# Optimization experiments

Measured on AMD Instinct MI355X. Metric: run time of the kernel, lower is better.

The kernel has to match this reference:

```python
import jax, jax.numpy as jnp
from jax import lax
import numpy as np

B, T, D = 16, 4096, 512          # batch, encoder length, d_model
C, FW = 10, 100                  # aconv_chans, aconv_filts (kernel width 2*FW+1)
SHARP = 2.0                      # sharpening_factor


def setup_inputs() -> dict:
    key = jax.random.key(0)
    ks = jax.random.split(key, 11)
    s = 1.0 / np.sqrt(D)
    sc = 1.0 / np.sqrt(2 * FW + 1)
    return {
        "value": jax.random.normal(ks[0], (B, T, D), jnp.float32),
        "query": jax.random.normal(ks[1], (B, D), jnp.float32),
        "input_lengths": jax.random.randint(ks[2], (B,), T // 2, T + 1),
        "att_prev": jax.random.uniform(ks[3], (B, T), jnp.float32),
        # learned parameters (torch Linear stores W as [out,in]; y = x @ W.T + b)
        "W_enc": jax.random.uniform(ks[4], (D, D), jnp.float32, -s, s),
        "b_enc": jax.random.uniform(ks[5], (D,), jnp.float32, -s, s),
        "W_dec": jax.random.uniform(ks[6], (D, D), jnp.float32, -s, s),
        "W_att": jax.random.uniform(ks[7], (D, C), jnp.float32, -s, s),
        "W_conv": jax.random.uniform(ks[8], (C, 1, 2 * FW + 1), jnp.float32, -sc, sc),
        "w_g": jax.random.uniform(ks[9], (1, D), jnp.float32, -s, s),
        "b_g": jax.random.uniform(ks[10], (1,), jnp.float32, -s, s),
    }


def reference(value, query, input_lengths, att_prev,
              W_enc, b_enc, W_dec, W_att, W_conv, w_g, b_g):
    # pre_compute_enc_h = mlp_enc(enc_h): [B,T,D]
    pre_enc = jnp.einsum('btd,ed->bte', value, W_enc) + b_enc
    # dec_z_tiled = mlp_dec(dec_z): [B,1,D]
    dec_tiled = (query @ W_dec.T)[:, None, :]
    # loc_conv: 1D conv over T, in_ch=1 -> out_ch=C, same padding -> [B,C,T]
    conv = lax.conv_general_dilated(att_prev[:, None, :], W_conv,
                                    window_strides=(1,), padding=[(FW, FW)],
                                    dimension_numbers=('NCH', 'OIH', 'NCH'))
    # mlp_att on transposed conv: [B,T,C] @ W_att.T -> [B,T,D]
    att_conv = jnp.einsum('bct,dc->btd', conv, W_att)
    # e = gvec(tanh(sum)): [B,T]
    e = jnp.einsum('btd,d->bt', jnp.tanh(att_conv + pre_enc + dec_tiled), w_g[0]) + b_g[0]
    # pad mask: positions >= length are masked to -inf (use large finite neg)
    pad_mask = jnp.arange(T)[None, :] >= input_lengths[:, None]
    e = jnp.where(pad_mask, -1e30, e)
    att_weights = jax.nn.softmax(SHARP * e, axis=1)            # [B,T]
    context = jnp.einsum('btd,bt->bd', value, att_weights)     # [B,D]
    return context, att_weights
```

## Files before the change

### kernel.cpp

```cpp
#include <hip/hip_runtime.h>
#include <hip/hip_bf16.h>

constexpr int kB  = 16;
constexpr int kT  = 4096;
constexpr int kD  = 512;
constexpr int kC  = 10;
constexpr int kFW = 100;
constexpr int kKW = 2 * kFW + 1;
constexpr int kKP = 544;

typedef __attribute__((ext_vector_type(8))) short short8_t;
typedef __attribute__((ext_vector_type(4))) float float4_t;

__device__ __forceinline__ float tanh_fast(float x) {
  float ax = fabsf(x);
  float z  = __expf(-2.0f * ax);
  float r  = (1.0f - z) / (1.0f + z);
  return copysignf(r, x);
}

__device__ __forceinline__ short f2bf(float x) {
  unsigned u = __float_as_uint(x);
  u += 0x7fffu + ((u >> 16) & 1u);
  return (short)(u >> 16);
}

__device__ __forceinline__ unsigned pk2(float lo, float hi) {
  __hip_bfloat162 h = __float22bfloat162_rn(make_float2(lo, hi));
  union { __hip_bfloat162 h2; unsigned u; } cv; cv.h2 = h; return cv.u;
}

__device__ __forceinline__ float bf2f(short s) {
  return __uint_as_float(((unsigned)(unsigned short)s) << 16);
}

__device__ __forceinline__ void glds16(const void* g, void* l) {
  __builtin_amdgcn_global_load_lds(
      (const __attribute__((address_space(1))) void*)g,
      (__attribute__((address_space(3))) void*)l, 16, 0, 0);
}

__global__ __launch_bounds__(256) void prep_kernel(
    const float* __restrict__ query, const float* __restrict__ W_dec,
    const float* __restrict__ b_enc, float* __restrict__ bias,
    const float* __restrict__ W_enc, const float* __restrict__ W_att,
    short* __restrict__ Wbf,
    const float* __restrict__ att_prev, const float* __restrict__ W_conv,
    const float* __restrict__ value, const int* __restrict__ lens,
    short* __restrict__ Abf) {
  __shared__ float ap[256 + 2 * kFW];
  __shared__ float wc[kC * kKW];
  int blk = blockIdx.x;
  int tid = threadIdx.x;

  if (blk < 2048) {
    int gw   = (blk * 256 + tid) >> 6;
    int lane = tid & 63;
    int b = gw >> 9, d = gw & (kD - 1);
    const float* q = query + (size_t)b * kD;
    const float* w = W_dec + (size_t)d * kD;
    float s = 0.f;
#pragma unroll
    for (int k0 = 0; k0 < kD; k0 += 256) {
      float4 qa = *(const float4*)(q + k0 + lane * 4);
      float4 wa = *(const float4*)(w + k0 + lane * 4);
      s += qa.x * wa.x + qa.y * wa.y + qa.z * wa.z + qa.w * wa.w;
    }
#pragma unroll
    for (int off = 32; off > 0; off >>= 1) s += __shfl_down(s, off, 64);
    if (lane == 0) bias[gw] = b_enc[d] + s;
  } else if (blk < 2048 + 512) {
    int d = blk - 2048;
    for (int c = tid; c < kKP; c += 256) {
      float v = 0.f;
      if (c < kD)           v = W_enc[(size_t)d * kD + c];
      else if (c < kD + kC) v = W_att[(size_t)d * kC + (c - kD)];
      Wbf[(size_t)d * kKP + c] = f2bf(v);
    }
  } else if (blk < 2048 + 512 + 256) {
    int lin = blk - 2560;
    int b = lin >> 4, t0 = (lin & 15) * 256;
    for (int i = tid; i < kC * kKW; i += 256) wc[i] = W_conv[i];
    for (int i = tid; i < 256 + 2 * kFW; i += 256) {
      int p = t0 - kFW + i;
      ap[i] = (p >= 0 && p < kT) ? att_prev[(size_t)b * kT + p] : 0.f;
    }
    __syncthreads();
    float acc[kC];
#pragma unroll
    for (int c = 0; c < kC; ++c) acc[c] = 0.f;
    for (int j = 0; j < kKW; ++j) {
      float a = ap[tid + j];
#pragma unroll
      for (int c = 0; c < kC; ++c) acc[c] += a * wc[c * kKW + j];
    }
    unsigned ow[16];
#pragma unroll
    for (int i = 0; i < 5; ++i) ow[i] = pk2(acc[2 * i], acc[2 * i + 1]);
#pragma unroll
    for (int i = 5; i < 16; ++i) ow[i] = 0u;
    uint4* out = (uint4*)(Abf + ((size_t)b * kT + t0 + tid) * kKP + kD);
#pragma unroll
    for (int i = 0; i < 4; ++i)
      out[i] = make_uint4(ow[4 * i], ow[4 * i + 1], ow[4 * i + 2], ow[4 * i + 3]);
  } else {
    int lin = blk - 2816;
    int b = lin >> 6, t0 = (lin & 63) * 64;
    if (t0 >= lens[b]) return;
    const float* src = value + ((size_t)b * kT + t0) * kD;
    short* dst = Abf + ((size_t)b * kT + t0) * kKP;
#pragma unroll
    for (int i = 0; i < 16; ++i) {
      int c = tid + i * 256;
      int row = c >> 6, col = (c & 63) * 8;
      float4 f0 = *(const float4*)(src + (size_t)row * kD + col);
      float4 f1 = *(const float4*)(src + (size_t)row * kD + col + 4);
      uint4 o;
      o.x = pk2(f0.x, f0.y); o.y = pk2(f0.z, f0.w);
      o.z = pk2(f1.x, f1.y); o.w = pk2(f1.z, f1.w);
      *(uint4*)(dst + (size_t)row * kKP + col) = o;
    }
  }
}

__global__ __launch_bounds__(256, 2) void e_kernel(
    const short* __restrict__ Abf, const short* __restrict__ Wbf,
    const float* __restrict__ bias, const float* __restrict__ w_g,
    const int* __restrict__ lens, float* __restrict__ e_part) {
  __shared__ short As[3 * 256 * 32];
  __shared__ short Bs[3 * 128 * 32];

  int tid = threadIdx.x;
  int L    = blockIdx.x;
  int xcd  = L & 7;
  int slot = L >> 3;
  int bn   = slot & 3;
  int mt   = (slot >> 2) * 8 + xcd;
  int b  = mt >> 4;
  int t0 = (mt & 15) * 256;
  if (t0 >= lens[b]) return;
  int n0 = bn * 128;

  int w    = tid >> 6;
  int lane = tid & 63;
  int nl   = lane & 15;
  int quad = lane >> 4;
  int wm = w >> 1, wn = w & 1;

  int r4  = lane >> 2;
  int kc4 = (lane & 3) ^ (r4 & 3);
  const short* asrc = Abf + ((size_t)(b * kT + t0) + w * 64 + r4) * kKP + kc4 * 8;
  const short* bsrc = Wbf + (size_t)(n0 + w * 32 + r4) * kKP + kc4 * 8;

  int co = (quad ^ (nl & 3)) * 8;

  float4_t acc[8][4] = {};

#define STAGE(bi, k0)                                                   \
  do {                                                                  \
    short* ad = As + (bi) * 8192 + (w * 64) * 32;                       \
    short* bd = Bs + (bi) * 4096 + (w * 32) * 32;                       \
    const short* as_ = asrc + (k0);                                     \
    const short* bs_ = bsrc + (k0);                                     \
    glds16(as_,                ad);                                     \
    glds16(as_ + 16 * kKP,     ad + 16 * 32);                           \
    glds16(as_ + 32 * kKP,     ad + 32 * 32);                           \
    glds16(as_ + 48 * kKP,     ad + 48 * 32);                           \
    glds16(bs_,                bd);                                     \
    glds16(bs_ + 16 * kKP,     bd + 16 * 32);                           \
  } while (0)

  STAGE(0, 0);
  STAGE(1, 32);
  int cur = 0, stg = 2;
#pragma unroll 1
  for (int kk = 0; kk < 17; ++kk) {
    if (kk < 15) STAGE(stg, (kk + 2) * 32);
    if (kk < 15)      asm volatile("s_waitcnt vmcnt(12)" ::: "memory");
    else if (kk < 16) asm volatile("s_waitcnt vmcnt(6)" ::: "memory");
    else              asm volatile("s_waitcnt vmcnt(0)" ::: "memory");
    __builtin_amdgcn_s_barrier();
    __builtin_amdgcn_sched_barrier(0);
    const short* aB = As + cur * 8192 + (wm * 128 + nl) * 32 + co;
    const short* bB = Bs + cur * 4096 + (wn * 64 + nl) * 32 + co;
    short8_t a_frag[8], b_frag[4];
#pragma unroll
    for (int i = 0; i < 8; ++i) a_frag[i] = *(const short8_t*)(aB + i * 512);
#pragma unroll
    for (int j = 0; j < 4; ++j) b_frag[j] = *(const short8_t*)(bB + j * 512);
    __builtin_amdgcn_s_setprio(1);
#pragma unroll
    for (int i = 0; i < 8; ++i)
#pragma unroll
      for (int j = 0; j < 4; ++j)
        acc[i][j] = __builtin_amdgcn_mfma_f32_16x16x32_bf16(
            a_frag[i], b_frag[j], acc[i][j], 0, 0, 0);
    __builtin_amdgcn_s_setprio(0);
    __builtin_amdgcn_sched_barrier(0);
    __builtin_amdgcn_s_barrier();
    cur = (cur == 2) ? 0 : cur + 1;
    stg = (stg == 2) ? 0 : stg + 1;
  }
#undef STAGE

  float bias_r[4], wg_r[4];
#pragma unroll
  for (int j = 0; j < 4; ++j) {
    int d = n0 + wn * 64 + j * 16 + nl;
    bias_r[j] = bias[b * kD + d];
    wg_r[j]   = w_g[d];
  }
  int p = bn * 2 + wn;
  float* ep = e_part + ((size_t)p * kB + b) * kT + t0 + wm * 128;
#pragma unroll
  for (int i = 0; i < 8; ++i) {
#pragma unroll
    for (int r = 0; r < 4; ++r) {
      float s = 0.f;
#pragma unroll
      for (int j = 0; j < 4; ++j)
        s += wg_r[j] * tanh_fast(acc[i][j][r] + bias_r[j]);
      s += __shfl_xor(s, 1, 64);
      s += __shfl_xor(s, 2, 64);
      s += __shfl_xor(s, 4, 64);
      s += __shfl_xor(s, 8, 64);
      if (nl == 0) ep[i * 16 + quad * 4 + r] = s;
    }
  }
}

__global__ void softmax1_kernel(const float* __restrict__ e_part,
                                const int* __restrict__ lens,
                                float* __restrict__ eb,
                                float* __restrict__ stats,
                                float* __restrict__ ctx) {
  __shared__ float sred[256];
  int b = blockIdx.x >> 4, ch = blockIdx.x & 15;
  int tid = threadIdx.x;
  int len = lens[b];
  if (ch == 0) {
    ctx[b * kD + tid]       = 0.f;
    ctx[b * kD + 256 + tid] = 0.f;
  }
  int t = ch * 256 + tid;
  float v = -3.0e38f;
  if (t < len) {
    const float* ep = e_part + (size_t)b * kT + t;
    float s = 0.f;
#pragma unroll
    for (int p = 0; p < 8; ++p) s += ep[(size_t)p * kB * kT];
    eb[(size_t)b * kT + t] = s;
    v = s;
  }
  sred[tid] = v; __syncthreads();
  for (int s = 128; s > 0; s >>= 1) {
    if (tid < s) sred[tid] = fmaxf(sred[tid], sred[tid + s]);
    __syncthreads();
  }
  float m = sred[0]; __syncthreads();
  float l = (v > -1.0e38f) ? __expf(2.0f * (v - m)) : 0.f;
  sred[tid] = l; __syncthreads();
  for (int s = 128; s > 0; s >>= 1) {
    if (tid < s) sred[tid] += sred[tid + s];
    __syncthreads();
  }
  if (tid == 0) {
    stats[(b * 16 + ch) * 2]     = m;
    stats[(b * 16 + ch) * 2 + 1] = sred[0];
  }
}

__global__ void ctx_att_kernel(const float* __restrict__ eb,
                               const float* __restrict__ stats,
                               const int* __restrict__ lens,
                               const short* __restrict__ Abf,
                               float* __restrict__ att,
                               float* __restrict__ ctx) {
  __shared__ float red[4][kD];
  int b = blockIdx.y;
  int len = lens[b];
  int t0 = blockIdx.x * 64;
  int tid = threadIdx.x;
  float M = -3.0e38f;
#pragma unroll
  for (int p = 0; p < 16; ++p) M = fmaxf(M, stats[(b * 16 + p) * 2]);
  float Lsum = 0.f;
#pragma unroll
  for (int p = 0; p < 16; ++p) {
    float mc = stats[(b * 16 + p) * 2], lc = stats[(b * 16 + p) * 2 + 1];
    if (lc > 0.f) Lsum += lc * __expf(2.0f * (mc - M));
  }
  float inv = 1.0f / Lsum;
  const float* e = eb + (size_t)b * kT + t0;
  if (tid < 64) {
    int t = t0 + tid;
    att[(size_t)b * kT + t] = (t < len) ? __expf(2.0f * (e[tid] - M)) * inv : 0.0f;
  }
  if (t0 >= len) return;
  int w = tid >> 6, lane = tid & 63;
  int tb = w * 16;
  int tmax = min(16, len - t0 - tb);
  float a[8] = {0.f, 0.f, 0.f, 0.f, 0.f, 0.f, 0.f, 0.f};
  const short* vp = Abf + ((size_t)b * kT + t0 + tb) * kKP + lane * 8;
  for (int t = 0; t < tmax; ++t) {
    float wt = __expf(2.0f * (e[tb + t] - M)) * inv;
    short8_t v = *(const short8_t*)(vp + (size_t)t * kKP);
#pragma unroll
    for (int i = 0; i < 8; ++i) a[i] += wt * bf2f(v[i]);
  }
#pragma unroll
  for (int i = 0; i < 8; ++i) red[w][lane * 8 + i] = a[i];
  __syncthreads();
  for (int col = tid; col < kD; col += 256) {
    float s = red[0][col] + red[1][col] + red[2][col] + red[3][col];
    atomicAdd(&ctx[b * kD + col], s);
  }
}

extern "C" void kernel_launch(void* const* d_in, const int* in_sizes, int n_in,
                              void* d_out, int out_size, void* d_ws, size_t ws_size,
                              hipStream_t stream) {
  const float* value    = (const float*)d_in[0];
  const float* query    = (const float*)d_in[1];
  const int*   lens     = (const int*)  d_in[2];
  const float* att_prev = (const float*)d_in[3];
  const float* W_enc    = (const float*)d_in[4];
  const float* b_enc    = (const float*)d_in[5];
  const float* W_dec    = (const float*)d_in[6];
  const float* W_att    = (const float*)d_in[7];
  const float* W_conv   = (const float*)d_in[8];
  const float* w_g      = (const float*)d_in[9];

  float* ws     = (float*)d_ws;
  float* e_part = ws;
  float* eb     = e_part + (size_t)8 * kB * kT;
  float* stats  = eb + (size_t)kB * kT;
  float* bias   = stats + 512;
  short* Wbf    = (short*)(bias + (size_t)kB * kD);
  short* Abf    = Wbf + (size_t)kD * kKP;
  float* ctx = (float*)d_out;
  float* att = ctx + (size_t)kB * kD;

  prep_kernel<<<3840, 256, 0, stream>>>(query, W_dec, b_enc, bias,
                                        W_enc, W_att, Wbf,
                                        att_prev, W_conv, value, lens, Abf);
  e_kernel<<<1024, 256, 0, stream>>>(Abf, Wbf, bias, w_g, lens, e_part);
  softmax1_kernel<<<kB * 16, 256, 0, stream>>>(e_part, lens, eb, stats, ctx);
  ctx_att_kernel<<<dim3(kT / 64, kB), 256, 0, stream>>>(eb, stats, lens, Abf, att, ctx);
}
```

Baseline: 306.1 us.

## Restructure e_kernel GEMM into 256x256 tiles with 8-wave ping-pong pipeline

Enlarges the e_kernel tile from 256x128 with 4 waves to 256x256 with 8 waves, using a K-step of 64 with double buffering and an XOR swizzle over 8 chunks. Each K tile is split into four quadrant MFMA phases interleaved with staging and barriers, in the style of a ping-pong schedule. K padding grows from 544 to 576 so the K dimension divides into 64-wide steps, and the conv-feature writes are widened to zero the extra columns. The aim is more reuse per LDS load and better overlap of global-to-LDS copies with MFMA. The cost is more LDS (128KB), heavier register pressure, and extra zero padding in the GEMM.

```diff
diff --git a/kernel.cpp b/kernel.cpp
--- a/kernel.cpp
+++ b/kernel.cpp
@@ -7,7 +7,7 @@
 constexpr int kC  = 10;
 constexpr int kFW = 100;
 constexpr int kKW = 2 * kFW + 1;
-constexpr int kKP = 544;
+constexpr int kKP = 576;
 
 typedef __attribute__((ext_vector_type(8))) short short8_t;
 typedef __attribute__((ext_vector_type(4))) float float4_t;
@@ -94,14 +94,14 @@
 #pragma unroll
       for (int c = 0; c < kC; ++c) acc[c] += a * wc[c * kKW + j];
     }
-    unsigned ow[16];
+    unsigned ow[32];
 #pragma unroll
     for (int i = 0; i < 5; ++i) ow[i] = pk2(acc[2 * i], acc[2 * i + 1]);
 #pragma unroll
-    for (int i = 5; i < 16; ++i) ow[i] = 0u;
+    for (int i = 5; i < 32; ++i) ow[i] = 0u;
     uint4* out = (uint4*)(Abf + ((size_t)b * kT + t0 + tid) * kKP + kD);
 #pragma unroll
-    for (int i = 0; i < 4; ++i)
+    for (int i = 0; i < 8; ++i)
       out[i] = make_uint4(ow[4 * i], ow[4 * i + 1], ow[4 * i + 2], ow[4 * i + 3]);
   } else {
     int lin = blk - 2816;
@@ -123,85 +123,126 @@
   }
 }
 
-__global__ __launch_bounds__(256, 2) void e_kernel(
+__global__ __launch_bounds__(512, 2) void e_kernel(
     const short* __restrict__ Abf, const short* __restrict__ Wbf,
     const float* __restrict__ bias, const float* __restrict__ w_g,
     const int* __restrict__ lens, float* __restrict__ e_part) {
-  __shared__ short As[3 * 256 * 32];
-  __shared__ short Bs[3 * 128 * 32];
-
-  int tid = threadIdx.x;
+  __shared__ short As[2 * 256 * 64];
+  __shared__ short Bs[2 * 256 * 64];
+
+  int tid  = threadIdx.x;
   int L    = blockIdx.x;
-  int xcd  = L & 7;
-  int slot = L >> 3;
-  int bn   = slot & 3;
-  int mt   = (slot >> 2) * 8 + xcd;
+  int g    = (L & 7) * 64 + (L >> 3);
+  int mt   = g >> 1;
+  int bn   = g & 1;
   int b  = mt >> 4;
   int t0 = (mt & 15) * 256;
   if (t0 >= lens[b]) return;
-  int n0 = bn * 128;
+  int n0 = bn * 256;
 
   int w    = tid >> 6;
   int lane = tid & 63;
   int nl   = lane & 15;
   int quad = lane >> 4;
-  int wm = w >> 1, wn = w & 1;
-
-  int r4  = lane >> 2;
-  int kc4 = (lane & 3) ^ (r4 & 3);
-  const short* asrc = Abf + ((size_t)(b * kT + t0) + w * 64 + r4) * kKP + kc4 * 8;
-  const short* bsrc = Wbf + (size_t)(n0 + w * 32 + r4) * kKP + kc4 * 8;
-
-  int co = (quad ^ (nl & 3)) * 8;
-
+  int wm = w >> 2, wn = w & 3;
+
+  int srow = w * 8 + (lane >> 3);
+  int sc   = (lane & 7) ^ ((lane >> 3) & 7);
+  const short* aS = Abf + ((size_t)(b * kT + t0) + srow) * kKP + sc * 8;
+  const short* bS = Wbf + ((size_t)(n0 + srow)) * kKP + sc * 8;
+
+  int x7  = nl & 7;
+  int co0 = ((0 * 4 + quad) ^ x7) * 8;
+  int co1 = ((1 * 4 + quad) ^ x7) * 8;
+
+  short8_t aF[8], bF0[4], bF1[4];
   float4_t acc[8][4] = {};
 
-#define STAGE(bi, k0)                                                   \
-  do {                                                                  \
-    short* ad = As + (bi) * 8192 + (w * 64) * 32;                       \
-    short* bd = Bs + (bi) * 4096 + (w * 32) * 32;                       \
-    const short* as_ = asrc + (k0);                                     \
-    const short* bs_ = bsrc + (k0);                                     \
-    glds16(as_,                ad);                                     \
-    glds16(as_ + 16 * kKP,     ad + 16 * 32);                           \
-    glds16(as_ + 32 * kKP,     ad + 32 * 32);                           \
-    glds16(as_ + 48 * kKP,     ad + 48 * 32);                           \
-    glds16(bs_,                bd);                                     \
-    glds16(bs_ + 16 * kKP,     bd + 16 * 32);                           \
-  } while (0)
-
-  STAGE(0, 0);
-  STAGE(1, 32);
-  int cur = 0, stg = 2;
+#define BARM() asm volatile("s_barrier" ::: "memory")
+#define VMW(n) asm volatile("s_waitcnt vmcnt(" #n ")" ::: "memory")
+
+#define STAGE_A(NXT, H, TAU)                                                \
+  do {                                                                      \
+    glds16(aS + (size_t)((H) * 128) * kKP + (TAU) * 64,                     \
+           &As[(NXT) * 16384 + ((H) * 128 + w * 8) * 64]);                  \
+    glds16(aS + (size_t)((H) * 128 + 64) * kKP + (TAU) * 64,                \
+           &As[(NXT) * 16384 + ((H) * 128 + 64 + w * 8) * 64]);             \
+  } while (0)
+#define STAGE_B(NXT, H, TAU)                                                \
+  do {                                                                      \
+    glds16(bS + (size_t)((H) * 128) * kKP + (TAU) * 64,                     \
+           &Bs[(NXT) * 16384 + ((H) * 128 + w * 8) * 64]);                  \
+    glds16(bS + (size_t)((H) * 128 + 64) * kKP + (TAU) * 64,                \
+           &Bs[(NXT) * 16384 + ((H) * 128 + 64 + w * 8) * 64]);             \
+  } while (0)
+
+#define LOAD_A(CUR, MH)                                                     \
+  do {                                                                      \
+    const short* p_ = &As[(CUR) * 16384 + (wm * 128 + (MH) * 64 + nl) * 64];\
+    _Pragma("unroll") for (int fi = 0; fi < 4; ++fi) {                      \
+      aF[fi * 2 + 0] = *(const short8_t*)(p_ + fi * 1024 + co0);            \
+      aF[fi * 2 + 1] = *(const short8_t*)(p_ + fi * 1024 + co1);            \
+    }                                                                       \
+  } while (0)
+#define LOAD_B(CUR, NH, DST)                                                \
+  do {                                                                      \
+    const short* p_ = &Bs[(CUR) * 16384 + (wn * 64 + (NH) * 32 + nl) * 64]; \
+    _Pragma("unroll") for (int fj = 0; fj < 2; ++fj) {                      \
+      DST[fj * 2 + 0] = *(const short8_t*)(p_ + fj * 1024 + co0);           \
+      DST[fj * 2 + 1] = *(const short8_t*)(p_ + fj * 1024 + co1);           \
+    }                                                                       \
+  } while (0)
+
+#define MFMA_Q(MH, NH, BFR)                                                 \
+  do {                                                                      \
+    __builtin_amdgcn_s_setprio(1);                                          \
+    _Pragma("unroll") for (int fi = 0; fi < 4; ++fi)                        \
+      _Pragma("unroll") for (int fj = 0; fj < 2; ++fj)                      \
+        _Pragma("unroll") for (int ks = 0; ks < 2; ++ks)                    \
+          acc[(MH) * 4 + fi][(NH) * 2 + fj] =                               \
+              __builtin_amdgcn_mfma_f32_16x16x32_bf16(                      \
+                  aF[fi * 2 + ks], BFR[fj * 2 + ks],                        \
+                  acc[(MH) * 4 + fi][(NH) * 2 + fj], 0, 0, 0);              \
+    __builtin_amdgcn_s_setprio(0);                                          \
+  } while (0)
+
+#define TILE(CUR, NXT, TAU, DO_STAGE, WAIT1, WAIT3)                         \
+  do {                                                                      \
+                                                    \
+    LOAD_A(CUR, 0); LOAD_B(CUR, 0, bF0);                                    \
+    if (DO_STAGE) STAGE_A(NXT, 0, TAU);                                     \
+    BARM(); MFMA_Q(0, 0, bF0); BARM();                                      \
+                                                    \
+    LOAD_B(CUR, 1, bF1);                                                    \
+    if (DO_STAGE) STAGE_B(NXT, 0, TAU);                                     \
+    WAIT1; BARM(); MFMA_Q(0, 1, bF1); BARM();                               \
+                                                    \
+    LOAD_A(CUR, 1);                                                         \
+    if (DO_STAGE) STAGE_B(NXT, 1, TAU);                                     \
+    BARM(); MFMA_Q(1, 0, bF0); BARM();                                      \
+                                                    \
+    if (DO_STAGE) STAGE_A(NXT, 1, TAU);                                     \
+    WAIT3; BARM(); MFMA_Q(1, 1, bF1); BARM();                               \
+  } while (0)
+
+  STAGE_A(0, 0, 0); STAGE_B(0, 0, 0); STAGE_B(0, 1, 0); STAGE_A(0, 1, 0);
+  VMW(2); BARM();
+
 #pragma unroll 1
-  for (int kk = 0; kk < 17; ++kk) {
-    if (kk < 15) STAGE(stg, (kk + 2) * 32);
-    if (kk < 15)      asm volatile("s_waitcnt vmcnt(12)" ::: "memory");
-    else if (kk < 16) asm volatile("s_waitcnt vmcnt(6)" ::: "memory");
-    else              asm volatile("s_waitcnt vmcnt(0)" ::: "memory");
-    __builtin_amdgcn_s_barrier();
-    __builtin_amdgcn_sched_barrier(0);
-    const short* aB = As + cur * 8192 + (wm * 128 + nl) * 32 + co;
-    const short* bB = Bs + cur * 4096 + (wn * 64 + nl) * 32 + co;
-    short8_t a_frag[8], b_frag[4];
-#pragma unroll
-    for (int i = 0; i < 8; ++i) a_frag[i] = *(const short8_t*)(aB + i * 512);
-#pragma unroll
-    for (int j = 0; j < 4; ++j) b_frag[j] = *(const short8_t*)(bB + j * 512);
-    __builtin_amdgcn_s_setprio(1);
-#pragma unroll
-    for (int i = 0; i < 8; ++i)
-#pragma unroll
-      for (int j = 0; j < 4; ++j)
-        acc[i][j] = __builtin_amdgcn_mfma_f32_16x16x32_bf16(
-            a_frag[i], b_frag[j], acc[i][j], 0, 0, 0);
-    __builtin_amdgcn_s_setprio(0);
-    __builtin_amdgcn_sched_barrier(0);
-    __builtin_amdgcn_s_barrier();
-    cur = (cur == 2) ? 0 : cur + 1;
-    stg = (stg == 2) ? 0 : stg + 1;
-  }
-#undef STAGE
+  for (int tp = 0; tp < 4; ++tp) {
+    TILE(0, 1, 2 * tp + 1, 1, VMW(4), VMW(2));
+    TILE(1, 0, 2 * tp + 2, 1, VMW(4), VMW(2));
+  }
+  TILE(0, 1, 0, 0, VMW(0), (void)0);
+
+#undef TILE
+#undef MFMA_Q
+#undef LOAD_B
+#undef LOAD_A
+#undef STAGE_B
+#undef STAGE_A
+#undef VMW
+#undef BARM
 
   float bias_r[4], wg_r[4];
 #pragma unroll
@@ -210,7 +251,7 @@
     bias_r[j] = bias[b * kD + d];
     wg_r[j]   = w_g[d];
   }
-  int p = bn * 2 + wn;
+  int p = bn * 4 + wn;
   float* ep = e_part + ((size_t)p * kB + b) * kT + t0 + wm * 128;
 #pragma unroll
   for (int i = 0; i < 8; ++i) {
@@ -344,7 +385,7 @@
   prep_kernel<<<3840, 256, 0, stream>>>(query, W_dec, b_enc, bias,
                                         W_enc, W_att, Wbf,
                                         att_prev, W_conv, value, lens, Abf);
-  e_kernel<<<1024, 256, 0, stream>>>(Abf, Wbf, bias, w_g, lens, e_part);
+  e_kernel<<<512, 512, 0, stream>>>(Abf, Wbf, bias, w_g, lens, e_part);
   softmax1_kernel<<<kB * 16, 256, 0, stream>>>(e_part, lens, eb, stats, ctx);
   ctx_att_kernel<<<dim3(kT / 64, kB), 256, 0, stream>>>(eb, stats, lens, Abf, att, ctx);
 }
```

New measurement: 293.0 us. -4.3%, faster.
